# Kernel tuning notes

Hardware: AMD Instinct MI355X
Metric: run time of the kernel (lower is better)

Reference implementation:

```python
import jax, jax.numpy as jnp
import numpy as np

NEG_SLOPE = 0.2

def gat_conv(x, edge_index, W, att_src, att_dst, bias, heads, out_dim):
    """PyG-style GATConv with add_self_loops=True, concat=True.
    x: [N, F_in]; edge_index: [2, E] with row 0 = src, row 1 = dst.
    W: [F_in, heads*out_dim]; att_src/att_dst: [heads, out_dim]; bias: [heads*out_dim].
    """
    N = x.shape[0]
    loop = jnp.arange(N)
    src = jnp.concatenate([edge_index[0], loop])  # [E+N]
    dst = jnp.concatenate([edge_index[1], loop])

    h = (x @ W).reshape(N, heads, out_dim)              # [N, H, D]
    a_s = jnp.sum(h * att_src[None], axis=-1)           # [N, H]
    a_d = jnp.sum(h * att_dst[None], axis=-1)           # [N, H]

    e = a_s[src] + a_d[dst]                             # [E+N, H]
    e = jax.nn.leaky_relu(e, NEG_SLOPE)
    # segment softmax over incoming edges of each dst node
    e_max = jax.ops.segment_max(e, dst, num_segments=N)  # [N, H]
    ex = jnp.exp(e - e_max[dst])
    denom = jax.ops.segment_sum(ex, dst, num_segments=N)  # [N, H] (>0: self loops)
    alpha = ex / denom[dst]                              # [E+N, H]

    msg = h[src] * alpha[..., None]                      # [E+N, H, D]
    out = jax.ops.segment_sum(msg, dst, num_segments=N)  # [N, H, D]
    return out.reshape(N, heads * out_dim) + bias


def setup_inputs() -> dict:
    key = jax.random.key(0)
    ks = jax.random.split(key, 16)
    N, F_in, D, H = 50000, 165, 64, 4
    E = 800000
    x = jax.random.normal(ks[0], (N, F_in), dtype=jnp.float32)
    edge_index = jax.random.randint(ks[1], (2, E), 0, N, dtype=jnp.int64)

    def glorot(k, shape):
        lim = float(np.sqrt(6.0 / (shape[0] + shape[-1])))
        return jax.random.uniform(k, shape, jnp.float32, -lim, lim)

    return {
        "x": x,
        "edge_index": edge_index,
        "proj_W": glorot(ks[2], (F_in, D)),
        "proj_b": jnp.zeros((D,), jnp.float32),
        "W1": glorot(ks[3], (D, H * D)),
        "att_src1": glorot(ks[4], (H, D)),
        "att_dst1": glorot(ks[5], (H, D)),
        "b1": jnp.zeros((H * D,), jnp.float32),
        "W2": glorot(ks[6], (H * D, D)),
        "att_src2": glorot(ks[7], (1, D)),
        "att_dst2": glorot(ks[8], (1, D)),
        "b2": jnp.zeros((D,), jnp.float32),
        "cls_W": glorot(ks[9], (D, 1)),
        "cls_b": jnp.zeros((1,), jnp.float32),
    }


def reference(x, edge_index, proj_W, proj_b, W1, att_src1, att_dst1, b1,
              W2, att_src2, att_dst2, b2, cls_W, cls_b):
    D = proj_W.shape[1]
    h = jax.nn.relu(x @ proj_W + proj_b)                              # [N, 64]
    h = jax.nn.relu(gat_conv(h, edge_index, W1, att_src1, att_dst1, b1, 4, D))   # [N, 256]
    h = jax.nn.relu(gat_conv(h, edge_index, W2, att_src2, att_dst2, b2, 1, D))   # [N, 64]
    return jnp.squeeze(h @ cls_W + cls_b, axis=-1)                    # [N]
```

## Files before the change

### kernel.cpp

```cpp
#include <hip/hip_runtime.h>

#define F_IN 165
#define KP_PROJ 168
constexpr float NEG_SLOPE = 0.2f;

__device__ __forceinline__ float lrelu(float z) { return fmaxf(z, NEG_SLOPE * z); }

__global__ void k_trans(const float* __restrict__ pw, const float* __restrict__ w2,
                        const float* __restrict__ w1, const float* __restrict__ as1w,
                        const float* __restrict__ ad1w,
                        float* __restrict__ t0, float* __restrict__ t2,
                        float* __restrict__ va, int* __restrict__ dc, int ndc) {
    int i = blockIdx.x * 256 + threadIdx.x;
    const int n0 = 64 * KP_PROJ, n2 = 64 * 256;
    if (i < n0) {
        int c = i / KP_PROJ, r = i - c * KP_PROJ;
        t0[i] = (r < F_IN) ? pw[r * 64 + c] : 0.f;
    } else if (i < n0 + n2) {
        int j = i - n0; int c = j >> 8, r = j & 255;
        t2[j] = w2[r * 64 + c];
    } else if (i < n0 + n2 + 512) {
        int j = i - n0 - n2;
        int i2 = j >> 6;
        int plane = i2 >> 2, h = i2 & 3, k = j & 63;
        const float* att = plane ? ad1w : as1w;
        float acc = 0.f;
        for (int c = 0; c < 64; ++c)
            acc = fmaf(w1[k * 256 + h * 64 + c], att[h * 64 + c], acc);
        va[j] = acc;
    }
    int z = i - (n0 + n2 + 512);
    if (z >= 0 && z < ndc) dc[z] = 0;
}

__global__ void k_proj(const float* __restrict__ x, const float* __restrict__ Wt,
                       const float* __restrict__ b, const float* __restrict__ va,
                       float* __restrict__ h0, float* __restrict__ as_,
                       float* __restrict__ ad_, int N) {
    __shared__ float xs[32][KP_PROJ];
    __shared__ float vas[8][65];
    __shared__ float hrow[4][64];
    int base = blockIdx.x * 32;
    int t = threadIdx.x;
    for (int idx = t; idx < 512; idx += 256)
        vas[idx >> 6][idx & 63] = va[idx];
    for (int idx = t; idx < 32 * KP_PROJ; idx += 256) {
        int nl = idx / KP_PROJ, k = idx - nl * KP_PROJ;
        int node = base + nl;
        xs[nl][k] = (node < N && k < F_IN) ? x[(size_t)node * F_IN + k] : 0.f;
    }
    __syncthreads();
    int g = t >> 6, col = t & 63;
    float acc[8];
    float bb = b[col];
#pragma unroll
    for (int m = 0; m < 8; ++m) acc[m] = bb;
    const float* wrow = Wt + col * KP_PROJ;
    for (int k4 = 0; k4 < KP_PROJ / 4; ++k4) {
        float4 wv = *(const float4*)(wrow + k4 * 4);
#pragma unroll
        for (int m = 0; m < 8; ++m) {
            float4 av = *(const float4*)&xs[g * 8 + m][k4 * 4];
            acc[m] = fmaf(av.x, wv.x, acc[m]);
            acc[m] = fmaf(av.y, wv.y, acc[m]);
            acc[m] = fmaf(av.z, wv.z, acc[m]);
            acc[m] = fmaf(av.w, wv.w, acc[m]);
        }
    }
    int i8 = col & 7, c8 = col >> 3;
    const float* vbase = &vas[i8][c8 * 8];
    const float* hbase = &hrow[g][c8 * 8];
#pragma unroll
    for (int m = 0; m < 8; ++m) {
        int node = base + g * 8 + m;
        float h = fmaxf(acc[m], 0.f);
        if (node < N) h0[(size_t)node * 64 + col] = h;
        hrow[g][col] = h;
        float r = 0.f;
#pragma unroll
        for (int e = 0; e < 8; ++e)
            r = fmaf(hbase[e], vbase[e], r);
        r += __shfl_xor(r, 8, 64);
        r += __shfl_xor(r, 16, 64);
        r += __shfl_xor(r, 32, 64);
        if (node < N && col < 8) {
            if (col < 4) as_[(size_t)node * 4 + col] = r;
            else         ad_[(size_t)node * 4 + (col - 4)] = r;
        }
    }
}

__global__ void k_lin2(const float* __restrict__ h1, const float* __restrict__ Wt,
                       const float* __restrict__ att_s, const float* __restrict__ att_d,
                       float* __restrict__ out, float* __restrict__ as_,
                       float* __restrict__ ad_, int N) {
    __shared__ float hs[32][256];
    int base = blockIdx.x * 32;
    int t = threadIdx.x;
    for (int i = 0; i < 8; ++i) {
        int idx4 = t + i * 256;
        int nl = idx4 >> 6, k4 = idx4 & 63;
        int node = base + nl;
        float4 v = make_float4(0.f, 0.f, 0.f, 0.f);
        if (node < N) v = *(const float4*)(h1 + (size_t)node * 256 + k4 * 4);
        *(float4*)&hs[nl][k4 * 4] = v;
    }
    __syncthreads();
    int g = t >> 6, col = t & 63;
    float acc[8] = {};
    const float* wrow = Wt + col * 256;
    for (int k4 = 0; k4 < 64; ++k4) {
        float4 wv = *(const float4*)(wrow + k4 * 4);
#pragma unroll
        for (int m = 0; m < 8; ++m) {
            float4 av = *(const float4*)&hs[g * 8 + m][k4 * 4];
            acc[m] = fmaf(av.x, wv.x, acc[m]);
            acc[m] = fmaf(av.y, wv.y, acc[m]);
            acc[m] = fmaf(av.z, wv.z, acc[m]);
            acc[m] = fmaf(av.w, wv.w, acc[m]);
        }
    }
    float sw = att_s[col], dw = att_d[col];
#pragma unroll
    for (int m = 0; m < 8; ++m) {
        int node = base + g * 8 + m;
        if (node < N) out[(size_t)node * 64 + col] = acc[m];
        float sv = acc[m] * sw, dv = acc[m] * dw;
#pragma unroll
        for (int off = 32; off; off >>= 1) {
            sv += __shfl_xor(sv, off, 64);
            dv += __shfl_xor(dv, off, 64);
        }
        if (col == 0 && node < N) { as_[node] = sv; ad_[node] = dv; }
    }
}

__global__ void k_deg(const int* __restrict__ ei, int E, int* __restrict__ deg) {
    for (int i = blockIdx.x * blockDim.x + threadIdx.x; i < E; i += gridDim.x * blockDim.x) {
        atomicAdd(&deg[ei[E + i]], 1);
    }
}

__global__ void k_scan_part(const int* __restrict__ deg, int* __restrict__ out,
                            int* __restrict__ partials, int n) {
    __shared__ int tmp[1024];
    int b = blockIdx.x, t = threadIdx.x;
    int i = b * 1024 + t;
    int v = (i < n) ? deg[i] : 0;
    tmp[t] = v;
    __syncthreads();
    for (int off = 1; off < 1024; off <<= 1) {
        int xval = (t >= off) ? tmp[t - off] : 0;
        __syncthreads();
        tmp[t] += xval;
        __syncthreads();
    }
    if (i < n) out[i] = tmp[t] - v;
    if (t == 1023) partials[b] = tmp[t];
}

__global__ void k_scan_small(int* __restrict__ partials, int nblk) {
    int lane = threadIdx.x & 63;
    int carry = 0;
    for (int base = 0; base < nblk; base += 64) {
        int idx = base + lane;
        int v = (idx < nblk) ? partials[idx] : 0;
        int orig = v;
#pragma unroll
        for (int off = 1; off < 64; off <<= 1) {
            int u = __shfl_up(v, off, 64);
            if (lane >= off) v += u;
        }
        if (idx < nblk) partials[idx] = carry + v - orig;
        carry += __shfl(v, 63, 64);
    }
}

__global__ void k_scan_add(int* __restrict__ rowptr, const int* __restrict__ partials,
                           int n, int total) {
    int i = blockIdx.x * 1024 + threadIdx.x;
    if (i < n) rowptr[i] += partials[blockIdx.x];
    if (i == 0) rowptr[n] = total;
}

__global__ void k_scatter(const int* __restrict__ ei, int E,
                          const int* __restrict__ rowptr, int* __restrict__ cursor,
                          int* __restrict__ csrc) {
    for (int i = blockIdx.x * blockDim.x + threadIdx.x; i < E; i += gridDim.x * blockDim.x) {
        int src = ei[i], dst = ei[E + i];
        int pos = rowptr[dst] + atomicAdd(&cursor[dst], 1);
        csrc[pos] = src;
    }
}

__global__ void k_gat1f(const float* __restrict__ h0, const float* __restrict__ as1,
                        const float* __restrict__ ad1, const int* __restrict__ rowptr,
                        const int* __restrict__ csrc, const float* __restrict__ W1,
                        const float* __restrict__ b1, float* __restrict__ h1out, int N) {
    __shared__ float agg[4][256];
    int t = threadIdx.x, wv = t >> 6, lane = t & 63;
    int slot = lane >> 4, sl = lane & 15;
    int d = blockIdx.x * 4 + wv;
    if (d < N) {
        int s0 = rowptr[d], e0 = rowptr[d + 1];
        float4 ad = *(const float4*)(ad1 + (size_t)d * 4);
        float a00=0,a01=0,a02=0,a03=0;
        float a10=0,a11=0,a12=0,a13=0;
        float a20=0,a21=0,a22=0,a23=0;
        float a30=0,a31=0,a32=0,a33=0;
        float d0=0,d1=0,d2=0,d3=0;
        const float* hb = h0 + sl * 4;
        if (slot == 0) {
            float4 a = *(const float4*)(as1 + (size_t)d * 4);
            float wx = __expf(lrelu(a.x + ad.x));
            float wy = __expf(lrelu(a.y + ad.y));
            float wz = __expf(lrelu(a.z + ad.z));
            float ww = __expf(lrelu(a.w + ad.w));
            float4 hv = *(const float4*)(hb + (size_t)d * 64);
            a00 = wx*hv.x; a01 = wx*hv.y; a02 = wx*hv.z; a03 = wx*hv.w;
            a10 = wy*hv.x; a11 = wy*hv.y; a12 = wy*hv.z; a13 = wy*hv.w;
            a20 = wz*hv.x; a21 = wz*hv.y; a22 = wz*hv.z; a23 = wz*hv.w;
            a30 = ww*hv.x; a31 = ww*hv.y; a32 = ww*hv.z; a33 = ww*hv.w;
            d0 = wx; d1 = wy; d2 = wz; d3 = ww;
        }
        int j = s0 + slot;
        for (; j + 4 < e0; j += 8) {
            int sA = csrc[j], sB = csrc[j + 4];
            float4 aA = *(const float4*)(as1 + (size_t)sA * 4);
            float4 aB = *(const float4*)(as1 + (size_t)sB * 4);
            float4 hA = *(const float4*)(hb + (size_t)sA * 64);
            float4 hB = *(const float4*)(hb + (size_t)sB * 64);
            float wxA = __expf(lrelu(aA.x + ad.x));
            float wyA = __expf(lrelu(aA.y + ad.y));
            float wzA = __expf(lrelu(aA.z + ad.z));
            float wwA = __expf(lrelu(aA.w + ad.w));
            float wxB = __expf(lrelu(aB.x + ad.x));
            float wyB = __expf(lrelu(aB.y + ad.y));
            float wzB = __expf(lrelu(aB.z + ad.z));
            float wwB = __expf(lrelu(aB.w + ad.w));
            a00 = fmaf(wxA, hA.x, a00); a01 = fmaf(wxA, hA.y, a01);
            a02 = fmaf(wxA, hA.z, a02); a03 = fmaf(wxA, hA.w, a03);
            a10 = fmaf(wyA, hA.x, a10); a11 = fmaf(wyA, hA.y, a11);
            a12 = fmaf(wyA, hA.z, a12); a13 = fmaf(wyA, hA.w, a13);
            a20 = fmaf(wzA, hA.x, a20); a21 = fmaf(wzA, hA.y, a21);
            a22 = fmaf(wzA, hA.z, a22); a23 = fmaf(wzA, hA.w, a23);
            a30 = fmaf(wwA, hA.x, a30); a31 = fmaf(wwA, hA.y, a31);
            a32 = fmaf(wwA, hA.z, a32); a33 = fmaf(wwA, hA.w, a33);
            d0 += wxA; d1 += wyA; d2 += wzA; d3 += wwA;
            a00 = fmaf(wxB, hB.x, a00); a01 = fmaf(wxB, hB.y, a01);
            a02 = fmaf(wxB, hB.z, a02); a03 = fmaf(wxB, hB.w, a03);
            a10 = fmaf(wyB, hB.x, a10); a11 = fmaf(wyB, hB.y, a11);
            a12 = fmaf(wyB, hB.z, a12); a13 = fmaf(wyB, hB.w, a13);
            a20 = fmaf(wzB, hB.x, a20); a21 = fmaf(wzB, hB.y, a21);
            a22 = fmaf(wzB, hB.z, a22); a23 = fmaf(wzB, hB.w, a23);
            a30 = fmaf(wwB, hB.x, a30); a31 = fmaf(wwB, hB.y, a31);
            a32 = fmaf(wwB, hB.z, a32); a33 = fmaf(wwB, hB.w, a33);
            d0 += wxB; d1 += wyB; d2 += wzB; d3 += wwB;
        }
        if (j < e0) {
            int s = csrc[j];
            float4 a = *(const float4*)(as1 + (size_t)s * 4);
            float4 hv = *(const float4*)(hb + (size_t)s * 64);
            float wx = __expf(lrelu(a.x + ad.x));
            float wy = __expf(lrelu(a.y + ad.y));
            float wz = __expf(lrelu(a.z + ad.z));
            float ww = __expf(lrelu(a.w + ad.w));
            a00 = fmaf(wx, hv.x, a00); a01 = fmaf(wx, hv.y, a01);
            a02 = fmaf(wx, hv.z, a02); a03 = fmaf(wx, hv.w, a03);
            a10 = fmaf(wy, hv.x, a10); a11 = fmaf(wy, hv.y, a11);
            a12 = fmaf(wy, hv.z, a12); a13 = fmaf(wy, hv.w, a13);
            a20 = fmaf(wz, hv.x, a20); a21 = fmaf(wz, hv.y, a21);
            a22 = fmaf(wz, hv.z, a22); a23 = fmaf(wz, hv.w, a23);
            a30 = fmaf(ww, hv.x, a30); a31 = fmaf(ww, hv.y, a31);
            a32 = fmaf(ww, hv.z, a32); a33 = fmaf(ww, hv.w, a33);
            d0 += wx; d1 += wy; d2 += wz; d3 += ww;
        }
#pragma unroll
        for (int off = 16; off <= 32; off <<= 1) {
            a00 += __shfl_xor(a00, off, 64); a01 += __shfl_xor(a01, off, 64);
            a02 += __shfl_xor(a02, off, 64); a03 += __shfl_xor(a03, off, 64);
            a10 += __shfl_xor(a10, off, 64); a11 += __shfl_xor(a11, off, 64);
            a12 += __shfl_xor(a12, off, 64); a13 += __shfl_xor(a13, off, 64);
            a20 += __shfl_xor(a20, off, 64); a21 += __shfl_xor(a21, off, 64);
            a22 += __shfl_xor(a22, off, 64); a23 += __shfl_xor(a23, off, 64);
            a30 += __shfl_xor(a30, off, 64); a31 += __shfl_xor(a31, off, 64);
            a32 += __shfl_xor(a32, off, 64); a33 += __shfl_xor(a33, off, 64);
            d0  += __shfl_xor(d0,  off, 64); d1  += __shfl_xor(d1,  off, 64);
            d2  += __shfl_xor(d2,  off, 64); d3  += __shfl_xor(d3,  off, 64);
        }
        if (slot == 0) {
            float i0 = 1.f / d0, i1 = 1.f / d1, i2 = 1.f / d2, i3 = 1.f / d3;
            *(float4*)&agg[wv][  0 + sl * 4] = make_float4(a00*i0, a01*i0, a02*i0, a03*i0);
            *(float4*)&agg[wv][ 64 + sl * 4] = make_float4(a10*i1, a11*i1, a12*i1, a13*i1);
            *(float4*)&agg[wv][128 + sl * 4] = make_float4(a20*i2, a21*i2, a22*i2, a23*i2);
            *(float4*)&agg[wv][192 + sl * 4] = make_float4(a30*i3, a31*i3, a32*i3, a33*i3);
        }
    }
    __syncthreads();
    int h = t >> 6;
    float o0 = 0.f, o1 = 0.f, o2 = 0.f, o3 = 0.f;
    for (int k = 0; k < 64; ++k) {
        float wv1 = W1[k * 256 + t];
        o0 = fmaf(agg[0][h * 64 + k], wv1, o0);
        o1 = fmaf(agg[1][h * 64 + k], wv1, o1);
        o2 = fmaf(agg[2][h * 64 + k], wv1, o2);
        o3 = fmaf(agg[3][h * 64 + k], wv1, o3);
    }
    float bb = b1[t];
    int base = blockIdx.x * 4;
    if (base + 0 < N) h1out[(size_t)(base + 0) * 256 + t] = fmaxf(o0 + bb, 0.f);
    if (base + 1 < N) h1out[(size_t)(base + 1) * 256 + t] = fmaxf(o1 + bb, 0.f);
    if (base + 2 < N) h1out[(size_t)(base + 2) * 256 + t] = fmaxf(o2 + bb, 0.f);
    if (base + 3 < N) h1out[(size_t)(base + 3) * 256 + t] = fmaxf(o3 + bb, 0.f);
}

__global__ void k_gat2(const float* __restrict__ hlin, const float* __restrict__ as2,
                       const float* __restrict__ ad2, const int* __restrict__ rowptr,
                       const int* __restrict__ csrc, const float* __restrict__ bias,
                       const float* __restrict__ clsW, const float* __restrict__ clsB,
                       float* __restrict__ out, int N) {
    int t = threadIdx.x, wv = t >> 6, lane = t & 63;
    int slot = lane >> 4, sl = lane & 15;
    int d = blockIdx.x * 4 + wv;
    if (d >= N) return;
    int s0 = rowptr[d], e0 = rowptr[d + 1];
    float add = ad2[d];
    float ax = 0.f, ay = 0.f, az = 0.f, aw = 0.f, den = 0.f;
    const float* hb = hlin + sl * 4;
    if (slot == 0) {
        float w = __expf(lrelu(as2[d] + add));
        float4 hv = *(const float4*)(hb + (size_t)d * 64);
        ax = w * hv.x; ay = w * hv.y; az = w * hv.z; aw = w * hv.w;
        den = w;
    }
    int j = s0 + slot;
    for (; j + 4 < e0; j += 8) {
        int sA = csrc[j], sB = csrc[j + 4];
        float wA = __expf(lrelu(as2[sA] + add));
        float wB = __expf(lrelu(as2[sB] + add));
        float4 hA = *(const float4*)(hb + (size_t)sA * 64);
        float4 hB = *(const float4*)(hb + (size_t)sB * 64);
        ax = fmaf(wA, hA.x, ax); ay = fmaf(wA, hA.y, ay);
        az = fmaf(wA, hA.z, az); aw = fmaf(wA, hA.w, aw);
        den += wA;
        ax = fmaf(wB, hB.x, ax); ay = fmaf(wB, hB.y, ay);
        az = fmaf(wB, hB.z, az); aw = fmaf(wB, hB.w, aw);
        den += wB;
    }
    if (j < e0) {
        int s = csrc[j];
        float w = __expf(lrelu(as2[s] + add));
        float4 hv = *(const float4*)(hb + (size_t)s * 64);
        ax = fmaf(w, hv.x, ax); ay = fmaf(w, hv.y, ay);
        az = fmaf(w, hv.z, az); aw = fmaf(w, hv.w, aw);
        den += w;
    }
#pragma unroll
    for (int off = 16; off <= 32; off <<= 1) {
        ax += __shfl_xor(ax, off, 64); ay += __shfl_xor(ay, off, 64);
        az += __shfl_xor(az, off, 64); aw += __shfl_xor(aw, off, 64);
        den += __shfl_xor(den, off, 64);
    }
    float inv = 1.f / den;
    float4 bb = *(const float4*)(bias + sl * 4);
    float4 cw = *(const float4*)(clsW + sl * 4);
    float p = fmaxf(fmaf(ax, inv, bb.x), 0.f) * cw.x
            + fmaxf(fmaf(ay, inv, bb.y), 0.f) * cw.y
            + fmaxf(fmaf(az, inv, bb.z), 0.f) * cw.z
            + fmaxf(fmaf(aw, inv, bb.w), 0.f) * cw.w;
#pragma unroll
    for (int off = 1; off <= 8; off <<= 1) p += __shfl_xor(p, off, 64);
    if (lane == 0) out[d] = p + clsB[0];
}

extern "C" void kernel_launch(void* const* d_in, const int* in_sizes, int n_in,
                              void* d_out, int out_size, void* d_ws, size_t ws_size,
                              hipStream_t stream) {
    const float* x     = (const float*)d_in[0];
    const int*   ei    = (const int*)d_in[1];
    const float* projW = (const float*)d_in[2];
    const float* projB = (const float*)d_in[3];
    const float* W1    = (const float*)d_in[4];
    const float* as1w  = (const float*)d_in[5];
    const float* ad1w  = (const float*)d_in[6];
    const float* b1    = (const float*)d_in[7];
    const float* W2    = (const float*)d_in[8];
    const float* as2w  = (const float*)d_in[9];
    const float* ad2w  = (const float*)d_in[10];
    const float* b2    = (const float*)d_in[11];
    const float* clsW  = (const float*)d_in[12];
    const float* clsB  = (const float*)d_in[13];
    float* out = (float*)d_out;

    const int N = in_sizes[0] / F_IN;
    const int E = in_sizes[1] / 2;

    char* ws = (char*)d_ws;
    size_t off = 0;
    auto alloc = [&](size_t bytes) -> void* {
        void* p = ws + off;
        off += (bytes + 255) & ~(size_t)255;
        return p;
    };
    float* h0     = (float*)alloc((size_t)N * 64 * 4);
    float* h1     = (float*)alloc((size_t)N * 256 * 4);
    float* as1    = (float*)alloc((size_t)N * 4 * 4);
    float* ad1    = (float*)alloc((size_t)N * 4 * 4);
    float* as2    = (float*)alloc((size_t)N * 4);
    float* ad2    = (float*)alloc((size_t)N * 4);
    int*   dc     = (int*)alloc((size_t)2 * N * 4);
    int*   deg    = dc;
    int*   cursor = dc + N;
    int*   rowptr = (int*)alloc((size_t)(N + 1) * 4);
    int*   parts  = (int*)alloc(1024 * 4);
    int*   csrc   = (int*)alloc((size_t)E * 4);
    float* wt0    = (float*)alloc(64 * KP_PROJ * 4);
    float* wt2    = (float*)alloc(64 * 256 * 4);
    float* va     = (float*)alloc(512 * 4);
    float* h2lin  = h0;

    const int ntr = 64 * KP_PROJ + 64 * 256 + 512 + 2 * N;
    k_trans<<<(ntr + 255) / 256, 256, 0, stream>>>(
        projW, W2, W1, as1w, ad1w, wt0, wt2, va, dc, 2 * N);

    k_deg<<<1024, 256, 0, stream>>>(ei, E, deg);
    int nblk = (N + 1023) / 1024;
    k_scan_part<<<nblk, 1024, 0, stream>>>(deg, rowptr, parts, N);
    k_scan_small<<<1, 64, 0, stream>>>(parts, nblk);
    k_scan_add<<<nblk, 1024, 0, stream>>>(rowptr, parts, N, E);
    k_scatter<<<1024, 256, 0, stream>>>(ei, E, rowptr, cursor, csrc);

    k_proj<<<(N + 31) / 32, 256, 0, stream>>>(x, wt0, projB, va, h0, as1, ad1, N);

    k_gat1f<<<(N + 3) / 4, 256, 0, stream>>>(h0, as1, ad1, rowptr, csrc, W1, b1, h1, N);

    k_lin2<<<(N + 31) / 32, 256, 0, stream>>>(h1, wt2, as2w, ad2w, h2lin, as2, ad2, N);
    k_gat2<<<(N + 3) / 4, 256, 0, stream>>>(h2lin, as2, ad2, rowptr, csrc, b2,
                                            clsW, clsB, out, N);
}
```

Measured before the change: 303.4 us.

## Fold degree counting into transpose kernel, use wave-shuffle scan, unroll GAT2 gather

Degree counting moves into the weight-transpose kernel, and the zeroing of the degree and cursor arrays becomes an async memset. This removes one launch. The block scan now uses wavefront shuffle prefix sums with a small shared-memory pass instead of a barrier-heavy log-step shared-memory scan. The layer-2 aggregation loop processes four edges per iteration per slot instead of two, giving more independent gathers in flight at the cost of more registers. The remainder loop is rewritten to handle up to three leftover edges.

```diff
diff --git a/kernel.cpp b/kernel.cpp
--- a/kernel.cpp
+++ b/kernel.cpp
@@ -10,7 +10,8 @@
                         const float* __restrict__ w1, const float* __restrict__ as1w,
                         const float* __restrict__ ad1w,
                         float* __restrict__ t0, float* __restrict__ t2,
-                        float* __restrict__ va, int* __restrict__ dc, int ndc) {
+                        float* __restrict__ va,
+                        const int* __restrict__ ei, int E, int* __restrict__ deg) {
     int i = blockIdx.x * 256 + threadIdx.x;
     const int n0 = 64 * KP_PROJ, n2 = 64 * 256;
     if (i < n0) {
@@ -30,7 +31,7 @@
         va[j] = acc;
     }
     int z = i - (n0 + n2 + 512);
-    if (z >= 0 && z < ndc) dc[z] = 0;
+    if (z >= 0 && z < E) atomicAdd(&deg[ei[E + z]], 1);
 }
 
 __global__ void k_proj(const float* __restrict__ x, const float* __restrict__ Wt,
@@ -135,28 +136,34 @@
     }
 }
 
-__global__ void k_deg(const int* __restrict__ ei, int E, int* __restrict__ deg) {
-    for (int i = blockIdx.x * blockDim.x + threadIdx.x; i < E; i += gridDim.x * blockDim.x) {
-        atomicAdd(&deg[ei[E + i]], 1);
-    }
-}
-
 __global__ void k_scan_part(const int* __restrict__ deg, int* __restrict__ out,
                             int* __restrict__ partials, int n) {
-    __shared__ int tmp[1024];
+    __shared__ int wsum[16];
     int b = blockIdx.x, t = threadIdx.x;
+    int wv = t >> 6, lane = t & 63;
     int i = b * 1024 + t;
     int v = (i < n) ? deg[i] : 0;
-    tmp[t] = v;
+    int s = v;
+#pragma unroll
+    for (int off = 1; off < 64; off <<= 1) {
+        int u = __shfl_up(s, off, 64);
+        if (lane >= off) s += u;
+    }
+    if (lane == 63) wsum[wv] = s;
     __syncthreads();
-    for (int off = 1; off < 1024; off <<= 1) {
-        int xval = (t >= off) ? tmp[t - off] : 0;
-        __syncthreads();
-        tmp[t] += xval;
-        __syncthreads();
-    }
-    if (i < n) out[i] = tmp[t] - v;
-    if (t == 1023) partials[b] = tmp[t];
+    if (wv == 0) {
+        int ws = (lane < 16) ? wsum[lane] : 0;
+#pragma unroll
+        for (int off = 1; off < 16; off <<= 1) {
+            int u = __shfl_up(ws, off, 64);
+            if (lane >= off) ws += u;
+        }
+        if (lane < 16) wsum[lane] = ws;
+    }
+    __syncthreads();
+    int wbase = (wv == 0) ? 0 : wsum[wv - 1];
+    if (i < n) out[i] = wbase + s - v;
+    if (t == 1023) partials[b] = wsum[15];
 }
 
 __global__ void k_scan_small(int* __restrict__ partials, int nblk) {
@@ -334,20 +341,27 @@
         den = w;
     }
     int j = s0 + slot;
-    for (; j + 4 < e0; j += 8) {
-        int sA = csrc[j], sB = csrc[j + 4];
+    for (; j + 12 < e0; j += 16) {
+        int sA = csrc[j], sB = csrc[j + 4], sC = csrc[j + 8], sD = csrc[j + 12];
         float wA = __expf(lrelu(as2[sA] + add));
         float wB = __expf(lrelu(as2[sB] + add));
+        float wC = __expf(lrelu(as2[sC] + add));
+        float wD = __expf(lrelu(as2[sD] + add));
         float4 hA = *(const float4*)(hb + (size_t)sA * 64);
         float4 hB = *(const float4*)(hb + (size_t)sB * 64);
+        float4 hC = *(const float4*)(hb + (size_t)sC * 64);
+        float4 hD = *(const float4*)(hb + (size_t)sD * 64);
         ax = fmaf(wA, hA.x, ax); ay = fmaf(wA, hA.y, ay);
         az = fmaf(wA, hA.z, az); aw = fmaf(wA, hA.w, aw);
-        den += wA;
         ax = fmaf(wB, hB.x, ax); ay = fmaf(wB, hB.y, ay);
         az = fmaf(wB, hB.z, az); aw = fmaf(wB, hB.w, aw);
-        den += wB;
-    }
-    if (j < e0) {
+        ax = fmaf(wC, hC.x, ax); ay = fmaf(wC, hC.y, ay);
+        az = fmaf(wC, hC.z, az); aw = fmaf(wC, hC.w, aw);
+        ax = fmaf(wD, hD.x, ax); ay = fmaf(wD, hD.y, ay);
+        az = fmaf(wD, hD.z, az); aw = fmaf(wD, hD.w, aw);
+        den += wA + wB + wC + wD;
+    }
+    for (; j < e0; j += 4) {
         int s = csrc[j];
         float w = __expf(lrelu(as2[s] + add));
         float4 hv = *(const float4*)(hb + (size_t)s * 64);
@@ -419,11 +433,11 @@
     float* va     = (float*)alloc(512 * 4);
     float* h2lin  = h0;
 
-    const int ntr = 64 * KP_PROJ + 64 * 256 + 512 + 2 * N;
+    hipMemsetAsync(dc, 0, (size_t)2 * N * 4, stream);
+    const int ntr = 64 * KP_PROJ + 64 * 256 + 512 + E;
     k_trans<<<(ntr + 255) / 256, 256, 0, stream>>>(
-        projW, W2, W1, as1w, ad1w, wt0, wt2, va, dc, 2 * N);
-
-    k_deg<<<1024, 256, 0, stream>>>(ei, E, deg);
+        projW, W2, W1, as1w, ad1w, wt0, wt2, va, ei, E, deg);
+
     int nblk = (N + 1023) / 1024;
     k_scan_part<<<nblk, 1024, 0, stream>>>(deg, rowptr, parts, N);
     k_scan_small<<<1, 64, 0, stream>>>(parts, nblk);
```

Result: no change. 308.9 us (+1.8%).

## Precompute per-edge attention exponentials in scatter kernel for GAT layer 1

Applied to the files above, without the earlier changes.

Moves the leaky-relu and exp edge-weight computation for the first GAT layer into the CSR scatter kernel, which now runs after the projection. The weights are written to a new E x 4 buffer in CSR order. The aggregation kernel then reads them contiguously instead of gathering as1[src] and recomputing exp. This trades redundant exp work and a random gather for an extra 12.8 MB write plus a read, and scatter now writes float4s to random positions.

```diff
diff --git a/kernel.cpp b/kernel.cpp
--- a/kernel.cpp
+++ b/kernel.cpp
@@ -185,25 +185,34 @@
 
 __global__ void k_scatter(const int* __restrict__ ei, int E,
                           const int* __restrict__ rowptr, int* __restrict__ cursor,
-                          int* __restrict__ csrc) {
+                          const float* __restrict__ as1, const float* __restrict__ ad1,
+                          int* __restrict__ csrc, float* __restrict__ wexp) {
     for (int i = blockIdx.x * blockDim.x + threadIdx.x; i < E; i += gridDim.x * blockDim.x) {
         int src = ei[i], dst = ei[E + i];
         int pos = rowptr[dst] + atomicAdd(&cursor[dst], 1);
         csrc[pos] = src;
-    }
-}
-
-__global__ void k_gat1f(const float* __restrict__ h0, const float* __restrict__ as1,
-                        const float* __restrict__ ad1, const int* __restrict__ rowptr,
-                        const int* __restrict__ csrc, const float* __restrict__ W1,
-                        const float* __restrict__ b1, float* __restrict__ h1out, int N) {
+        float4 a = *(const float4*)(as1 + (size_t)src * 4);
+        float4 b = *(const float4*)(ad1 + (size_t)dst * 4);
+        float4 w;
+        w.x = __expf(lrelu(a.x + b.x));
+        w.y = __expf(lrelu(a.y + b.y));
+        w.z = __expf(lrelu(a.z + b.z));
+        w.w = __expf(lrelu(a.w + b.w));
+        *(float4*)(wexp + (size_t)pos * 4) = w;
+    }
+}
+
+__global__ void k_gat1f(const float* __restrict__ h0, const float* __restrict__ wexp4,
+                        const float* __restrict__ as1, const float* __restrict__ ad1,
+                        const int* __restrict__ rowptr, const int* __restrict__ csrc,
+                        const float* __restrict__ W1, const float* __restrict__ b1,
+                        float* __restrict__ h1out, int N) {
     __shared__ float agg[4][256];
     int t = threadIdx.x, wv = t >> 6, lane = t & 63;
     int slot = lane >> 4, sl = lane & 15;
     int d = blockIdx.x * 4 + wv;
     if (d < N) {
         int s0 = rowptr[d], e0 = rowptr[d + 1];
-        float4 ad = *(const float4*)(ad1 + (size_t)d * 4);
         float a00=0,a01=0,a02=0,a03=0;
         float a10=0,a11=0,a12=0,a13=0;
         float a20=0,a21=0,a22=0,a23=0;
@@ -212,10 +221,11 @@
         const float* hb = h0 + sl * 4;
         if (slot == 0) {
             float4 a = *(const float4*)(as1 + (size_t)d * 4);
-            float wx = __expf(lrelu(a.x + ad.x));
-            float wy = __expf(lrelu(a.y + ad.y));
-            float wz = __expf(lrelu(a.z + ad.z));
-            float ww = __expf(lrelu(a.w + ad.w));
+            float4 b = *(const float4*)(ad1 + (size_t)d * 4);
+            float wx = __expf(lrelu(a.x + b.x));
+            float wy = __expf(lrelu(a.y + b.y));
+            float wz = __expf(lrelu(a.z + b.z));
+            float ww = __expf(lrelu(a.w + b.w));
             float4 hv = *(const float4*)(hb + (size_t)d * 64);
             a00 = wx*hv.x; a01 = wx*hv.y; a02 = wx*hv.z; a03 = wx*hv.w;
             a10 = wy*hv.x; a11 = wy*hv.y; a12 = wy*hv.z; a13 = wy*hv.w;
@@ -226,54 +236,42 @@
         int j = s0 + slot;
         for (; j + 4 < e0; j += 8) {
             int sA = csrc[j], sB = csrc[j + 4];
-            float4 aA = *(const float4*)(as1 + (size_t)sA * 4);
-            float4 aB = *(const float4*)(as1 + (size_t)sB * 4);
+            float4 wA = *(const float4*)(wexp4 + (size_t)j * 4);
+            float4 wB = *(const float4*)(wexp4 + (size_t)(j + 4) * 4);
             float4 hA = *(const float4*)(hb + (size_t)sA * 64);
             float4 hB = *(const float4*)(hb + (size_t)sB * 64);
-            float wxA = __expf(lrelu(aA.x + ad.x));
-            float wyA = __expf(lrelu(aA.y + ad.y));
-            float wzA = __expf(lrelu(aA.z + ad.z));
-            float wwA = __expf(lrelu(aA.w + ad.w));
-            float wxB = __expf(lrelu(aB.x + ad.x));
-            float wyB = __expf(lrelu(aB.y + ad.y));
-            float wzB = __expf(lrelu(aB.z + ad.z));
-            float wwB = __expf(lrelu(aB.w + ad.w));
-            a00 = fmaf(wxA, hA.x, a00); a01 = fmaf(wxA, hA.y, a01);
-            a02 = fmaf(wxA, hA.z, a02); a03 = fmaf(wxA, hA.w, a03);
-            a10 = fmaf(wyA, hA.x, a10); a11 = fmaf(wyA, hA.y, a11);
-            a12 = fmaf(wyA, hA.z, a12); a13 = fmaf(wyA, hA.w, a13);
-            a20 = fmaf(wzA, hA.x, a20); a21 = fmaf(wzA, hA.y, a21);
-            a22 = fmaf(wzA, hA.z, a22); a23 = fmaf(wzA, hA.w, a23);
-            a30 = fmaf(wwA, hA.x, a30); a31 = fmaf(wwA, hA.y, a31);
-            a32 = fmaf(wwA, hA.z, a32); a33 = fmaf(wwA, hA.w, a33);
-            d0 += wxA; d1 += wyA; d2 += wzA; d3 += wwA;
-            a00 = fmaf(wxB, hB.x, a00); a01 = fmaf(wxB, hB.y, a01);
-            a02 = fmaf(wxB, hB.z, a02); a03 = fmaf(wxB, hB.w, a03);
-            a10 = fmaf(wyB, hB.x, a10); a11 = fmaf(wyB, hB.y, a11);
-            a12 = fmaf(wyB, hB.z, a12); a13 = fmaf(wyB, hB.w, a13);
-            a20 = fmaf(wzB, hB.x, a20); a21 = fmaf(wzB, hB.y, a21);
-            a22 = fmaf(wzB, hB.z, a22); a23 = fmaf(wzB, hB.w, a23);
-            a30 = fmaf(wwB, hB.x, a30); a31 = fmaf(wwB, hB.y, a31);
-            a32 = fmaf(wwB, hB.z, a32); a33 = fmaf(wwB, hB.w, a33);
-            d0 += wxB; d1 += wyB; d2 += wzB; d3 += wwB;
+            a00 = fmaf(wA.x, hA.x, a00); a01 = fmaf(wA.x, hA.y, a01);
+            a02 = fmaf(wA.x, hA.z, a02); a03 = fmaf(wA.x, hA.w, a03);
+            a10 = fmaf(wA.y, hA.x, a10); a11 = fmaf(wA.y, hA.y, a11);
+            a12 = fmaf(wA.y, hA.z, a12); a13 = fmaf(wA.y, hA.w, a13);
+            a20 = fmaf(wA.z, hA.x, a20); a21 = fmaf(wA.z, hA.y, a21);
+            a22 = fmaf(wA.z, hA.z, a22); a23 = fmaf(wA.z, hA.w, a23);
+            a30 = fmaf(wA.w, hA.x, a30); a31 = fmaf(wA.w, hA.y, a31);
+            a32 = fmaf(wA.w, hA.z, a32); a33 = fmaf(wA.w, hA.w, a33);
+            d0 += wA.x; d1 += wA.y; d2 += wA.z; d3 += wA.w;
+            a00 = fmaf(wB.x, hB.x, a00); a01 = fmaf(wB.x, hB.y, a01);
+            a02 = fmaf(wB.x, hB.z, a02); a03 = fmaf(wB.x, hB.w, a03);
+            a10 = fmaf(wB.y, hB.x, a10); a11 = fmaf(wB.y, hB.y, a11);
+            a12 = fmaf(wB.y, hB.z, a12); a13 = fmaf(wB.y, hB.w, a13);
+            a20 = fmaf(wB.z, hB.x, a20); a21 = fmaf(wB.z, hB.y, a21);
+            a22 = fmaf(wB.z, hB.z, a22); a23 = fmaf(wB.z, hB.w, a23);
+            a30 = fmaf(wB.w, hB.x, a30); a31 = fmaf(wB.w, hB.y, a31);
+            a32 = fmaf(wB.w, hB.z, a32); a33 = fmaf(wB.w, hB.w, a33);
+            d0 += wB.x; d1 += wB.y; d2 += wB.z; d3 += wB.w;
         }
         if (j < e0) {
             int s = csrc[j];
-            float4 a = *(const float4*)(as1 + (size_t)s * 4);
+            float4 w = *(const float4*)(wexp4 + (size_t)j * 4);
             float4 hv = *(const float4*)(hb + (size_t)s * 64);
-            float wx = __expf(lrelu(a.x + ad.x));
-            float wy = __expf(lrelu(a.y + ad.y));
-            float wz = __expf(lrelu(a.z + ad.z));
-            float ww = __expf(lrelu(a.w + ad.w));
-            a00 = fmaf(wx, hv.x, a00); a01 = fmaf(wx, hv.y, a01);
-            a02 = fmaf(wx, hv.z, a02); a03 = fmaf(wx, hv.w, a03);
-            a10 = fmaf(wy, hv.x, a10); a11 = fmaf(wy, hv.y, a11);
-            a12 = fmaf(wy, hv.z, a12); a13 = fmaf(wy, hv.w, a13);
-            a20 = fmaf(wz, hv.x, a20); a21 = fmaf(wz, hv.y, a21);
-            a22 = fmaf(wz, hv.z, a22); a23 = fmaf(wz, hv.w, a23);
-            a30 = fmaf(ww, hv.x, a30); a31 = fmaf(ww, hv.y, a31);
-            a32 = fmaf(ww, hv.z, a32); a33 = fmaf(ww, hv.w, a33);
-            d0 += wx; d1 += wy; d2 += wz; d3 += ww;
+            a00 = fmaf(w.x, hv.x, a00); a01 = fmaf(w.x, hv.y, a01);
+            a02 = fmaf(w.x, hv.z, a02); a03 = fmaf(w.x, hv.w, a03);
+            a10 = fmaf(w.y, hv.x, a10); a11 = fmaf(w.y, hv.y, a11);
+            a12 = fmaf(w.y, hv.z, a12); a13 = fmaf(w.y, hv.w, a13);
+            a20 = fmaf(w.z, hv.x, a20); a21 = fmaf(w.z, hv.y, a21);
+            a22 = fmaf(w.z, hv.z, a22); a23 = fmaf(w.z, hv.w, a23);
+            a30 = fmaf(w.w, hv.x, a30); a31 = fmaf(w.w, hv.y, a31);
+            a32 = fmaf(w.w, hv.z, a32); a33 = fmaf(w.w, hv.w, a33);
+            d0 += w.x; d1 += w.y; d2 += w.z; d3 += w.w;
         }
 #pragma unroll
         for (int off = 16; off <= 32; off <<= 1) {
@@ -414,6 +412,7 @@
     int*   rowptr = (int*)alloc((size_t)(N + 1) * 4);
     int*   parts  = (int*)alloc(1024 * 4);
     int*   csrc   = (int*)alloc((size_t)E * 4);
+    float* wexp1  = (float*)alloc((size_t)E * 4 * 4);
     float* wt0    = (float*)alloc(64 * KP_PROJ * 4);
     float* wt2    = (float*)alloc(64 * 256 * 4);
     float* va     = (float*)alloc(512 * 4);
@@ -428,11 +427,13 @@
     k_scan_part<<<nblk, 1024, 0, stream>>>(deg, rowptr, parts, N);
     k_scan_small<<<1, 64, 0, stream>>>(parts, nblk);
     k_scan_add<<<nblk, 1024, 0, stream>>>(rowptr, parts, N, E);
-    k_scatter<<<1024, 256, 0, stream>>>(ei, E, rowptr, cursor, csrc);
 
     k_proj<<<(N + 31) / 32, 256, 0, stream>>>(x, wt0, projB, va, h0, as1, ad1, N);
 
-    k_gat1f<<<(N + 3) / 4, 256, 0, stream>>>(h0, as1, ad1, rowptr, csrc, W1, b1, h1, N);
+    k_scatter<<<1024, 256, 0, stream>>>(ei, E, rowptr, cursor, as1, ad1, csrc, wexp1);
+
+    k_gat1f<<<(N + 3) / 4, 256, 0, stream>>>(h0, wexp1, as1, ad1, rowptr, csrc,
+                                             W1, b1, h1, N);
 
     k_lin2<<<(N + 31) / 32, 256, 0, stream>>>(h1, wt2, as2w, ad2w, h2lin, as2, ad2, N);
     k_gat2<<<(N + 3) / 4, 256, 0, stream>>>(h2lin, as2, ad2, rowptr, csrc, b2,
```

Result: no change. 301.8 us (-0.5%).
